# Performance work log

Hardware: AMD Instinct MI355X
Metric: run time of the kernel (lower is better)

Reference implementation:

```python
import jax, jax.numpy as jnp
import numpy as np

N = 131072
HIDDEN = 1024
MIN_STD = 1e-5
PRIOR_SIGMA1 = 4.0 / np.sqrt(1.0)
PRIOR_SIGMA2 = 2.25 / np.sqrt(float(HIDDEN))


def setup_inputs() -> dict:
    key = jax.random.key(0)
    ks = jax.random.split(key, 13)
    f = lambda k, shape: jax.random.normal(k, shape, dtype=jnp.float32)
    return {
        "x": f(ks[0], (N, 1)),
        "W1_mu": f(ks[1], (HIDDEN, 1)),
        "W1_rho": f(ks[2], (HIDDEN, 1)),
        "b1_mu": f(ks[3], (HIDDEN,)),
        "b1_rho": f(ks[4], (HIDDEN,)),
        "W2_mu": f(ks[5], (2, HIDDEN)),
        "W2_rho": f(ks[6], (2, HIDDEN)),
        "b2_mu": f(ks[7], (2,)),
        "b2_rho": f(ks[8], (2,)),
        "eps_W1": f(ks[9], (HIDDEN, 1)),
        "eps_b1": f(ks[10], (HIDDEN,)),
        "eps_W2": f(ks[11], (2, HIDDEN)),
        "eps_b2": f(ks[12], (2,)),
    }


def _kl(mu, sigma, prior_sigma):
    # KL( N(mu, sigma) || N(0, prior_sigma) ), summed over elements
    return 0.5 * jnp.sum(
        2.0 * jnp.log(prior_sigma / sigma) - 1.0
        + (sigma / prior_sigma) ** 2
        + (mu / prior_sigma) ** 2
    )


def _bbb_linear(x, W_mu, W_rho, b_mu, b_rho, eps_W, eps_b, prior_sigma):
    W_sigma = jax.nn.softplus(W_rho)
    b_sigma = jax.nn.softplus(b_rho)
    W = W_mu + W_sigma * eps_W  # [out, in]
    b = b_mu + b_sigma * eps_b  # [out]
    out = x @ W.T + b  # [N, out]
    kl = _kl(W_mu, W_sigma, prior_sigma) + _kl(b_mu, b_sigma, prior_sigma)
    return out, kl


def reference(x, W1_mu, W1_rho, b1_mu, b1_rho, W2_mu, W2_rho, b2_mu, b2_rho,
              eps_W1, eps_b1, eps_W2, eps_b2):
    h1, kl1 = _bbb_linear(x, W1_mu, W1_rho, b1_mu, b1_rho, eps_W1, eps_b1, PRIOR_SIGMA1)
    h3, kl3 = _bbb_linear(jax.nn.relu(h1), W2_mu, W2_rho, b2_mu, b2_rho, eps_W2, eps_b2, PRIOR_SIGMA2)
    means = h3[:, 0]
    stds = MIN_STD + jax.nn.softplus(h3[:, 1])
    kl = kl1 + kl3
    return means, stds, kl
```

## Files before the change

kernel.cpp:

```cpp
#include <hip/hip_runtime.h>
#include <math.h>

#define N_SAMPLES 131072
#define HIDDEN 1024

__device__ __forceinline__ float softplusf(float v) {
    return fmaxf(v, 0.0f) + log1pf(expf(-fabsf(v)));
}
__device__ __forceinline__ double softplusd(double v) {
    return fmax(v, 0.0) + log1p(exp(-fabs(v)));
}
__device__ __forceinline__ double kl_term(double mu, double sigma, double prior) {
    double r = sigma / prior;
    double m = mu / prior;
    return 0.5 * (-2.0 * log(r) - 1.0 + r * r + m * m);
}

__global__ __launch_bounds__(1024) void bbb_prep_kernel(
    const float* __restrict__ W1_mu, const float* __restrict__ W1_rho,
    const float* __restrict__ b1_mu, const float* __restrict__ b1_rho,
    const float* __restrict__ W2_mu, const float* __restrict__ W2_rho,
    const float* __restrict__ b2_mu, const float* __restrict__ b2_rho,
    const float* __restrict__ eps_W1, const float* __restrict__ eps_b1,
    const float* __restrict__ eps_W2, const float* __restrict__ eps_b2,
    float* __restrict__ t_out,
    float4* __restrict__ lut_out,
    float* __restrict__ kl_out)
{
    __shared__ float   s_key[HIDDEN];
    __shared__ int     s_perm[HIDDEN];
    __shared__ double  s_red[HIDDEN];
    __shared__ double4 s_d4[HIDDEN];
    __shared__ double4 s_base;

    const int tid = threadIdx.x;
    const double p1 = 4.0;
    const double p2 = 2.25 / 32.0;

    double w1  = (double)W1_mu[tid] + softplusd((double)W1_rho[tid]) * (double)eps_W1[tid];
    double bb1 = (double)b1_mu[tid] + softplusd((double)b1_rho[tid]) * (double)eps_b1[tid];
    double w2a = (double)W2_mu[tid]          + softplusd((double)W2_rho[tid])          * (double)eps_W2[tid];
    double w2b = (double)W2_mu[HIDDEN + tid] + softplusd((double)W2_rho[HIDDEN + tid]) * (double)eps_W2[HIDDEN + tid];

    double kl = 0.0;
    kl += kl_term((double)W1_mu[tid], softplusd((double)W1_rho[tid]), p1);
    kl += kl_term((double)b1_mu[tid], softplusd((double)b1_rho[tid]), p1);
    kl += kl_term((double)W2_mu[tid],          softplusd((double)W2_rho[tid]),          p2);
    kl += kl_term((double)W2_mu[HIDDEN + tid], softplusd((double)W2_rho[HIDDEN + tid]), p2);
    if (tid < 2) {
        kl += kl_term((double)b2_mu[tid], softplusd((double)b2_rho[tid]), p2);
    }
    s_red[tid] = kl;
    __syncthreads();
    for (int off = 512; off > 0; off >>= 1) {
        if (tid < off) s_red[tid] += s_red[tid + off];
        __syncthreads();
    }
    if (tid == 0) *kl_out = (float)s_red[0];

    double4 b4 = {0.0, 0.0, 0.0, 0.0};
    if (w1 < 0.0) {
        b4.x = w1 * w2a;  b4.y = bb1 * w2a;
        b4.z = w1 * w2b;  b4.w = bb1 * w2b;
    } else if (w1 == 0.0 && bb1 > 0.0) {
        b4.y = bb1 * w2a; b4.w = bb1 * w2b;
    }
    s_d4[tid] = b4;
    __syncthreads();
    for (int off = 512; off > 0; off >>= 1) {
        if (tid < off) {
            s_d4[tid].x += s_d4[tid + off].x;
            s_d4[tid].y += s_d4[tid + off].y;
            s_d4[tid].z += s_d4[tid + off].z;
            s_d4[tid].w += s_d4[tid + off].w;
        }
        __syncthreads();
    }
    if (tid == 0) {
        double bb2a = (double)b2_mu[0] + softplusd((double)b2_rho[0]) * (double)eps_b2[0];
        double bb2b = (double)b2_mu[1] + softplusd((double)b2_rho[1]) * (double)eps_b2[1];
        double4 sb;
        sb.x = s_d4[0].x;  sb.y = s_d4[0].y + bb2a;
        sb.z = s_d4[0].z;  sb.w = s_d4[0].w + bb2b;
        s_base = sb;
    }

    float key;
    if (w1 != 0.0) key = (float)(-bb1 / w1);
    else           key = __builtin_huge_valf();
    __syncthreads();
    s_key[tid]  = key;
    s_perm[tid] = tid;
    __syncthreads();

    for (int k = 2; k <= HIDDEN; k <<= 1) {
        for (int j = k >> 1; j > 0; j >>= 1) {
            int ixj = tid ^ j;
            if (ixj > tid) {
                bool up = ((tid & k) == 0);
                float a = s_key[tid], b = s_key[ixj];
                if ((a > b) == up) {
                    s_key[tid] = b; s_key[ixj] = a;
                    int pa = s_perm[tid];
                    s_perm[tid] = s_perm[ixj];
                    s_perm[ixj] = pa;
                }
            }
            __syncthreads();
        }
    }

    int jj = s_perm[tid];
    double w1s  = (double)W1_mu[jj] + softplusd((double)W1_rho[jj]) * (double)eps_W1[jj];
    double bb1s = (double)b1_mu[jj] + softplusd((double)b1_rho[jj]) * (double)eps_b1[jj];
    double w2as = (double)W2_mu[jj]          + softplusd((double)W2_rho[jj])          * (double)eps_W2[jj];
    double w2bs = (double)W2_mu[HIDDEN + jj] + softplusd((double)W2_rho[HIDDEN + jj]) * (double)eps_W2[HIDDEN + jj];

    double4 d4 = {0.0, 0.0, 0.0, 0.0};
    if (w1s > 0.0) {
        d4.x =  w1s * w2as;  d4.y =  bb1s * w2as;
        d4.z =  w1s * w2bs;  d4.w =  bb1s * w2bs;
    } else if (w1s < 0.0) {
        d4.x = -w1s * w2as;  d4.y = -bb1s * w2as;
        d4.z = -w1s * w2bs;  d4.w = -bb1s * w2bs;
    }
    __syncthreads();
    s_d4[tid] = d4;
    __syncthreads();

    for (int off = 1; off < HIDDEN; off <<= 1) {
        double4 v = s_d4[tid];
        if (tid >= off) {
            double4 u = s_d4[tid - off];
            v.x += u.x; v.y += u.y; v.z += u.z; v.w += u.w;
        }
        __syncthreads();
        s_d4[tid] = v;
        __syncthreads();
    }

    t_out[tid]          = s_key[tid];
    t_out[HIDDEN + tid] = __builtin_huge_valf();
    double4 pre = s_d4[tid];
    lut_out[tid + 1] = make_float4((float)(s_base.x + pre.x),
                                   (float)(s_base.y + pre.y),
                                   (float)(s_base.z + pre.z),
                                   (float)(s_base.w + pre.w));
    if (tid == 0) {
        lut_out[0] = make_float4((float)s_base.x, (float)s_base.y,
                                 (float)s_base.z, (float)s_base.w);
    }
}

__global__ __launch_bounds__(256) void bbb_eval_kernel(
    const float* __restrict__ x,
    const float* __restrict__ t_sorted,
    const float4* __restrict__ lut,
    float* __restrict__ means,
    float* __restrict__ stds)
{
    __shared__ float  s_t[2 * HIDDEN];
    __shared__ float4 s_lut[HIDDEN + 1];

    for (int i = threadIdx.x; i < 2 * HIDDEN; i += blockDim.x) s_t[i] = t_sorted[i];
    for (int i = threadIdx.x; i < HIDDEN + 1; i += blockDim.x) s_lut[i] = lut[i];
    __syncthreads();

    int gid = blockIdx.x * blockDim.x + threadIdx.x;
    float xv = x[gid];

    int idx = 0;
    #pragma unroll
    for (int s = HIDDEN; s > 0; s >>= 1) {
        idx += (s_t[idx + s - 1] <= xv) ? s : 0;
    }

    float4 c = s_lut[idx];
    float m = fmaf(xv, c.x, c.y);
    float u = fmaf(xv, c.z, c.w);
    means[gid] = m;
    stds[gid]  = 1e-5f + softplusf(u);
}

extern "C" void kernel_launch(void* const* d_in, const int* in_sizes, int n_in,
                              void* d_out, int out_size, void* d_ws, size_t ws_size,
                              hipStream_t stream) {
    const float* x      = (const float*)d_in[0];
    const float* W1_mu  = (const float*)d_in[1];
    const float* W1_rho = (const float*)d_in[2];
    const float* b1_mu  = (const float*)d_in[3];
    const float* b1_rho = (const float*)d_in[4];
    const float* W2_mu  = (const float*)d_in[5];
    const float* W2_rho = (const float*)d_in[6];
    const float* b2_mu  = (const float*)d_in[7];
    const float* b2_rho = (const float*)d_in[8];
    const float* eps_W1 = (const float*)d_in[9];
    const float* eps_b1 = (const float*)d_in[10];
    const float* eps_W2 = (const float*)d_in[11];
    const float* eps_b2 = (const float*)d_in[12];

    float* out = (float*)d_out;
    float*  t_ws   = (float*)d_ws;
    float4* lut_ws = (float4*)((char*)d_ws + 2 * HIDDEN * sizeof(float));

    bbb_prep_kernel<<<1, HIDDEN, 0, stream>>>(
        W1_mu, W1_rho, b1_mu, b1_rho, W2_mu, W2_rho, b2_mu, b2_rho,
        eps_W1, eps_b1, eps_W2, eps_b2,
        t_ws, lut_ws, out + 2 * N_SAMPLES);

    bbb_eval_kernel<<<N_SAMPLES / 256, 256, 0, stream>>>(
        x, t_ws, lut_ws, out, out + N_SAMPLES);
}
```

Measured before the change: 117.0 us.

## Replace sorted piecewise-linear lookup with direct per-sample hidden-layer evaluation

The prep kernel no longer sorts breakpoints or builds prefix-sum lookup tables in double precision. It now only writes per-unit sampled weights in float and reduces the KL term with wave shuffles. The eval kernel computes the full 1024-unit ReLU MLP for each sample directly, reading the parameters from global memory. This removes the serial sort and scan from the single-block prep kernel, but raises per-sample work from a binary search to about 3K FMAs.

```diff
diff --git a/kernel.cpp b/kernel.cpp
--- a/kernel.cpp
+++ b/kernel.cpp
@@ -7,179 +7,94 @@
 __device__ __forceinline__ float softplusf(float v) {
     return fmaxf(v, 0.0f) + log1pf(expf(-fabsf(v)));
 }
-__device__ __forceinline__ double softplusd(double v) {
-    return fmax(v, 0.0) + log1p(exp(-fabs(v)));
-}
-__device__ __forceinline__ double kl_term(double mu, double sigma, double prior) {
-    double r = sigma / prior;
-    double m = mu / prior;
-    return 0.5 * (-2.0 * log(r) - 1.0 + r * r + m * m);
+__device__ __forceinline__ float kl_term_f(float mu, float sigma, float inv_prior) {
+    float r = sigma * inv_prior;
+    float m = mu * inv_prior;
+    return 0.5f * (-2.0f * logf(r) - 1.0f + r * r + m * m);
 }
 
-__global__ __launch_bounds__(1024) void bbb_prep_kernel(
+__global__ __launch_bounds__(1024) void bbb_prep(
     const float* __restrict__ W1_mu, const float* __restrict__ W1_rho,
     const float* __restrict__ b1_mu, const float* __restrict__ b1_rho,
     const float* __restrict__ W2_mu, const float* __restrict__ W2_rho,
     const float* __restrict__ b2_mu, const float* __restrict__ b2_rho,
     const float* __restrict__ eps_W1, const float* __restrict__ eps_b1,
     const float* __restrict__ eps_W2, const float* __restrict__ eps_b2,
-    float* __restrict__ t_out,
-    float4* __restrict__ lut_out,
+    float4* __restrict__ params,
     float* __restrict__ kl_out)
 {
-    __shared__ float   s_key[HIDDEN];
-    __shared__ int     s_perm[HIDDEN];
-    __shared__ double  s_red[HIDDEN];
-    __shared__ double4 s_d4[HIDDEN];
-    __shared__ double4 s_base;
+    __shared__ double s_part[16];
+    const int tid = threadIdx.x;
 
-    const int tid = threadIdx.x;
-    const double p1 = 4.0;
-    const double p2 = 2.25 / 32.0;
+    const float ip1 = 0.25f;
+    const float ip2 = 32.0f / 2.25f;
 
-    double w1  = (double)W1_mu[tid] + softplusd((double)W1_rho[tid]) * (double)eps_W1[tid];
-    double bb1 = (double)b1_mu[tid] + softplusd((double)b1_rho[tid]) * (double)eps_b1[tid];
-    double w2a = (double)W2_mu[tid]          + softplusd((double)W2_rho[tid])          * (double)eps_W2[tid];
-    double w2b = (double)W2_mu[HIDDEN + tid] + softplusd((double)W2_rho[HIDDEN + tid]) * (double)eps_W2[HIDDEN + tid];
+    float w1mu  = W1_mu[tid],          w1rho  = W1_rho[tid];
+    float b1mu  = b1_mu[tid],          b1rho  = b1_rho[tid];
+    float w2amu = W2_mu[tid],          w2arho = W2_rho[tid];
+    float w2bmu = W2_mu[HIDDEN + tid], w2brho = W2_rho[HIDDEN + tid];
 
-    double kl = 0.0;
-    kl += kl_term((double)W1_mu[tid], softplusd((double)W1_rho[tid]), p1);
-    kl += kl_term((double)b1_mu[tid], softplusd((double)b1_rho[tid]), p1);
-    kl += kl_term((double)W2_mu[tid],          softplusd((double)W2_rho[tid]),          p2);
-    kl += kl_term((double)W2_mu[HIDDEN + tid], softplusd((double)W2_rho[HIDDEN + tid]), p2);
+    float sg_w1  = softplusf(w1rho);
+    float sg_b1  = softplusf(b1rho);
+    float sg_w2a = softplusf(w2arho);
+    float sg_w2b = softplusf(w2brho);
+
+    float w1  = fmaf(sg_w1,  eps_W1[tid],          w1mu);
+    float bb1 = fmaf(sg_b1,  eps_b1[tid],          b1mu);
+    float w2a = fmaf(sg_w2a, eps_W2[tid],          w2amu);
+    float w2b = fmaf(sg_w2b, eps_W2[HIDDEN + tid], w2bmu);
+
+    params[tid] = make_float4(w1, bb1, w2a, w2b);
+
+    double kl = (double)kl_term_f(w1mu,  sg_w1,  ip1)
+              + (double)kl_term_f(b1mu,  sg_b1,  ip1)
+              + (double)kl_term_f(w2amu, sg_w2a, ip2)
+              + (double)kl_term_f(w2bmu, sg_w2b, ip2);
+
     if (tid < 2) {
-        kl += kl_term((double)b2_mu[tid], softplusd((double)b2_rho[tid]), p2);
-    }
-    s_red[tid] = kl;
-    __syncthreads();
-    for (int off = 512; off > 0; off >>= 1) {
-        if (tid < off) s_red[tid] += s_red[tid + off];
-        __syncthreads();
-    }
-    if (tid == 0) *kl_out = (float)s_red[0];
-
-    double4 b4 = {0.0, 0.0, 0.0, 0.0};
-    if (w1 < 0.0) {
-        b4.x = w1 * w2a;  b4.y = bb1 * w2a;
-        b4.z = w1 * w2b;  b4.w = bb1 * w2b;
-    } else if (w1 == 0.0 && bb1 > 0.0) {
-        b4.y = bb1 * w2a; b4.w = bb1 * w2b;
-    }
-    s_d4[tid] = b4;
-    __syncthreads();
-    for (int off = 512; off > 0; off >>= 1) {
-        if (tid < off) {
-            s_d4[tid].x += s_d4[tid + off].x;
-            s_d4[tid].y += s_d4[tid + off].y;
-            s_d4[tid].z += s_d4[tid + off].z;
-            s_d4[tid].w += s_d4[tid + off].w;
-        }
-        __syncthreads();
+        kl += (double)kl_term_f(b2_mu[tid], softplusf(b2_rho[tid]), ip2);
     }
     if (tid == 0) {
-        double bb2a = (double)b2_mu[0] + softplusd((double)b2_rho[0]) * (double)eps_b2[0];
-        double bb2b = (double)b2_mu[1] + softplusd((double)b2_rho[1]) * (double)eps_b2[1];
-        double4 sb;
-        sb.x = s_d4[0].x;  sb.y = s_d4[0].y + bb2a;
-        sb.z = s_d4[0].z;  sb.w = s_d4[0].w + bb2b;
-        s_base = sb;
+        float bb2a = fmaf(softplusf(b2_rho[0]), eps_b2[0], b2_mu[0]);
+        float bb2b = fmaf(softplusf(b2_rho[1]), eps_b2[1], b2_mu[1]);
+        params[HIDDEN] = make_float4(bb2a, bb2b, 0.0f, 0.0f);
     }
 
-    float key;
-    if (w1 != 0.0) key = (float)(-bb1 / w1);
-    else           key = __builtin_huge_valf();
+    #pragma unroll
+    for (int off = 32; off > 0; off >>= 1) kl += __shfl_down(kl, off, 64);
+    if ((tid & 63) == 0) s_part[tid >> 6] = kl;
     __syncthreads();
-    s_key[tid]  = key;
-    s_perm[tid] = tid;
-    __syncthreads();
-
-    for (int k = 2; k <= HIDDEN; k <<= 1) {
-        for (int j = k >> 1; j > 0; j >>= 1) {
-            int ixj = tid ^ j;
-            if (ixj > tid) {
-                bool up = ((tid & k) == 0);
-                float a = s_key[tid], b = s_key[ixj];
-                if ((a > b) == up) {
-                    s_key[tid] = b; s_key[ixj] = a;
-                    int pa = s_perm[tid];
-                    s_perm[tid] = s_perm[ixj];
-                    s_perm[ixj] = pa;
-                }
-            }
-            __syncthreads();
-        }
-    }
-
-    int jj = s_perm[tid];
-    double w1s  = (double)W1_mu[jj] + softplusd((double)W1_rho[jj]) * (double)eps_W1[jj];
-    double bb1s = (double)b1_mu[jj] + softplusd((double)b1_rho[jj]) * (double)eps_b1[jj];
-    double w2as = (double)W2_mu[jj]          + softplusd((double)W2_rho[jj])          * (double)eps_W2[jj];
-    double w2bs = (double)W2_mu[HIDDEN + jj] + softplusd((double)W2_rho[HIDDEN + jj]) * (double)eps_W2[HIDDEN + jj];
-
-    double4 d4 = {0.0, 0.0, 0.0, 0.0};
-    if (w1s > 0.0) {
-        d4.x =  w1s * w2as;  d4.y =  bb1s * w2as;
-        d4.z =  w1s * w2bs;  d4.w =  bb1s * w2bs;
-    } else if (w1s < 0.0) {
-        d4.x = -w1s * w2as;  d4.y = -bb1s * w2as;
-        d4.z = -w1s * w2bs;  d4.w = -bb1s * w2bs;
-    }
-    __syncthreads();
-    s_d4[tid] = d4;
-    __syncthreads();
-
-    for (int off = 1; off < HIDDEN; off <<= 1) {
-        double4 v = s_d4[tid];
-        if (tid >= off) {
-            double4 u = s_d4[tid - off];
-            v.x += u.x; v.y += u.y; v.z += u.z; v.w += u.w;
-        }
-        __syncthreads();
-        s_d4[tid] = v;
-        __syncthreads();
-    }
-
-    t_out[tid]          = s_key[tid];
-    t_out[HIDDEN + tid] = __builtin_huge_valf();
-    double4 pre = s_d4[tid];
-    lut_out[tid + 1] = make_float4((float)(s_base.x + pre.x),
-                                   (float)(s_base.y + pre.y),
-                                   (float)(s_base.z + pre.z),
-                                   (float)(s_base.w + pre.w));
     if (tid == 0) {
-        lut_out[0] = make_float4((float)s_base.x, (float)s_base.y,
-                                 (float)s_base.z, (float)s_base.w);
+        double t = 0.0;
+        #pragma unroll
+        for (int i = 0; i < 16; ++i) t += s_part[i];
+        *kl_out = (float)t;
     }
 }
 
-__global__ __launch_bounds__(256) void bbb_eval_kernel(
+__global__ __launch_bounds__(256) void bbb_eval(
     const float* __restrict__ x,
-    const float* __restrict__ t_sorted,
-    const float4* __restrict__ lut,
+    const float4* __restrict__ params,
     float* __restrict__ means,
     float* __restrict__ stds)
 {
-    __shared__ float  s_t[2 * HIDDEN];
-    __shared__ float4 s_lut[HIDDEN + 1];
+    const int gid = blockIdx.x * blockDim.x + threadIdx.x;
+    const float xv = x[gid];
 
-    for (int i = threadIdx.x; i < 2 * HIDDEN; i += blockDim.x) s_t[i] = t_sorted[i];
-    for (int i = threadIdx.x; i < HIDDEN + 1; i += blockDim.x) s_lut[i] = lut[i];
-    __syncthreads();
+    const float4 b2 = params[HIDDEN];
+    float acc_a = b2.x;
+    float acc_b = b2.y;
 
-    int gid = blockIdx.x * blockDim.x + threadIdx.x;
-    float xv = x[gid];
-
-    int idx = 0;
-    #pragma unroll
-    for (int s = HIDDEN; s > 0; s >>= 1) {
-        idx += (s_t[idx + s - 1] <= xv) ? s : 0;
+    #pragma unroll 8
+    for (int j = 0; j < HIDDEN; ++j) {
+        float4 p = params[j];
+        float h = fmaxf(fmaf(p.x, xv, p.y), 0.0f);
+        acc_a = fmaf(h, p.z, acc_a);
+        acc_b = fmaf(h, p.w, acc_b);
     }
 
-    float4 c = s_lut[idx];
-    float m = fmaf(xv, c.x, c.y);
-    float u = fmaf(xv, c.z, c.w);
-    means[gid] = m;
-    stds[gid]  = 1e-5f + softplusf(u);
+    means[gid] = acc_a;
+    stds[gid]  = 1e-5f + softplusf(acc_b);
 }
 
 extern "C" void kernel_launch(void* const* d_in, const int* in_sizes, int n_in,
@@ -200,14 +115,13 @@
     const float* eps_b2 = (const float*)d_in[12];
 
     float* out = (float*)d_out;
-    float*  t_ws   = (float*)d_ws;
-    float4* lut_ws = (float4*)((char*)d_ws + 2 * HIDDEN * sizeof(float));
+    float4* params_ws = (float4*)d_ws;
 
-    bbb_prep_kernel<<<1, HIDDEN, 0, stream>>>(
+    bbb_prep<<<1, HIDDEN, 0, stream>>>(
         W1_mu, W1_rho, b1_mu, b1_rho, W2_mu, W2_rho, b2_mu, b2_rho,
         eps_W1, eps_b1, eps_W2, eps_b2,
-        t_ws, lut_ws, out + 2 * N_SAMPLES);
+        params_ws, out + 2 * N_SAMPLES);
 
-    bbb_eval_kernel<<<N_SAMPLES / 256, 256, 0, stream>>>(
-        x, t_ws, lut_ws, out, out + N_SAMPLES);
+    bbb_eval<<<N_SAMPLES / 256, 256, 0, stream>>>(
+        x, params_ws, out, out + N_SAMPLES);
 }
```

Result: slower. 124.6 us (+6.5%).
